# Kernel optimization log

Hardware: AMD Instinct MI355X
Metric: run time of the kernel (lower is better)

The kernel has to match this reference:

```python
import jax, jax.numpy as jnp
import numpy as np

N = 100000
E = 1600000
D_IN = 128
D_HID = 128
D_OUT = 128
HEADS = 4
NEG_SLOPE = 0.2  # PyG GATConv default leaky_relu slope


def setup_inputs() -> dict:
    key = jax.random.key(0)
    ks = jax.random.split(key, 16)
    ch1 = D_HID // HEADS
    ch2 = D_OUT // HEADS
    inp = {
        "x": jax.random.normal(ks[0], (N, D_IN), dtype=jnp.float32),
        "edge_index": jax.random.randint(ks[1], (2, E), 0, N, dtype=jnp.int64),
        # conv1 params
        "W1": jax.random.normal(ks[2], (D_IN, HEADS * ch1), dtype=jnp.float32) * 0.05,
        "a1_src": jax.random.normal(ks[3], (HEADS, ch1), dtype=jnp.float32) * 0.05,
        "a1_dst": jax.random.normal(ks[4], (HEADS, ch1), dtype=jnp.float32) * 0.05,
        "b1": jnp.zeros((HEADS * ch1,), dtype=jnp.float32),
        # conv2 params
        "W2": jax.random.normal(ks[5], (D_HID, HEADS * ch2), dtype=jnp.float32) * 0.05,
        "a2_src": jax.random.normal(ks[6], (HEADS, ch2), dtype=jnp.float32) * 0.05,
        "a2_dst": jax.random.normal(ks[7], (HEADS, ch2), dtype=jnp.float32) * 0.05,
        "b2": jnp.zeros((HEADS * ch2,), dtype=jnp.float32),
        # residual linear
        "Wr": jax.random.normal(ks[8], (D_IN, D_OUT), dtype=jnp.float32) * 0.05,
        "br": jnp.zeros((D_OUT,), dtype=jnp.float32),
    }
    return inp


def _gat_conv(x, W, a_src, a_dst, bias, src, dst, n_nodes):
    """Single PyG-style GATConv (concat heads, eval-mode / no dropout).
    src/dst already include self loops. x: [N, Din]. Returns [N, H*C]."""
    H, C = a_src.shape
    h = (x @ W).reshape(n_nodes, H, C)                      # [N,H,C]
    s_src = jnp.einsum("nhc,hc->nh", h, a_src)              # [N,H]
    s_dst = jnp.einsum("nhc,hc->nh", h, a_dst)              # [N,H]
    e = s_src[src] + s_dst[dst]                             # [E',H]
    e = jnp.where(e > 0, e, NEG_SLOPE * e)                  # leaky_relu
    # softmax over edges grouped by destination node
    e_max = jax.ops.segment_max(e, dst, num_segments=n_nodes)  # [N,H]
    e_exp = jnp.exp(e - e_max[dst])
    denom = jax.ops.segment_sum(e_exp, dst, num_segments=n_nodes)  # [N,H]
    alpha = e_exp / denom[dst]                              # [E',H]
    msg = alpha[:, :, None] * h[src]                        # [E',H,C]
    out = jax.ops.segment_sum(msg, dst, num_segments=n_nodes)  # [N,H,C]
    return out.reshape(n_nodes, H * C) + bias


def reference(x, edge_index, W1, a1_src, a1_dst, b1, W2, a2_src, a2_dst, b2, Wr, br):
    n_nodes = x.shape[0]
    loops = jnp.arange(n_nodes, dtype=edge_index.dtype)
    src = jnp.concatenate([edge_index[0], loops])           # add_self_loops=True
    dst = jnp.concatenate([edge_index[1], loops])
    h1 = _gat_conv(x, W1, a1_src, a1_dst, b1, src, dst, n_nodes)
    h1 = jax.nn.relu(h1)
    h2 = _gat_conv(h1, W2, a2_src, a2_dst, b2, src, dst, n_nodes)
    return h2 + x @ Wr + br
```

## Files before the change

### kernel.cpp

```cpp
#include <hip/hip_runtime.h>

#define NEG_SLOPE 0.2f

__device__ __forceinline__ float leaky1(float e) { return e > 0.f ? e : NEG_SLOPE * e; }

__device__ __forceinline__ unsigned short f2bf(float f) {
    unsigned u = __float_as_uint(f);
    u += 0x7fffu + ((u >> 16) & 1u);
    return (unsigned short)(u >> 16);
}

#define EPB 4096

__global__ __launch_bounds__(256) void bucket_hist(const int* __restrict__ dst,
                                                   int* __restrict__ gcnt,
                                                   int* __restrict__ relBase,
                                                   int E, int N, int NB) {
    __shared__ int hist[256];
    int t = threadIdx.x, blk = blockIdx.x;
    if (t < NB) hist[t] = 0;
    __syncthreads();
    int e0 = blk * EPB + t;
#pragma unroll 4
    for (int k = 0; k < EPB / 256; ++k) {
        int e = e0 + k * 256;
        if (e < E) {
            int d = dst[e];
            if ((unsigned)d < (unsigned)N) atomicAdd(&hist[d >> 9], 1);
        }
    }
    __syncthreads();
    if (t < NB) relBase[blk * NB + t] = atomicAdd(&gcnt[t], hist[t]);
}

__global__ __launch_bounds__(256) void scan_buckets(const int* __restrict__ gcnt,
                                                    int* __restrict__ gboff, int NB) {
    __shared__ int sm[256];
    int t = threadIdx.x;
    int v = (t < NB) ? gcnt[t] : 0;
    sm[t] = v;
    __syncthreads();
#pragma unroll
    for (int o = 1; o < 256; o <<= 1) {
        int u = (t >= o) ? sm[t - o] : 0;
        __syncthreads();
        sm[t] += u;
        __syncthreads();
    }
    if (t < NB) gboff[t] = sm[t] - v;
    if (t == NB - 1) gboff[NB] = sm[t];
}

__global__ __launch_bounds__(256) void bucket_scatter(const int* __restrict__ src,
                                                      const int* __restrict__ dst,
                                                      const int* __restrict__ gboff,
                                                      const int* __restrict__ relBase,
                                                      int2* __restrict__ eb,
                                                      int E, int N, int NB) {
    __shared__ int cur[256];
    int t = threadIdx.x, blk = blockIdx.x;
    if (t < NB) cur[t] = gboff[t] + relBase[blk * NB + t];
    __syncthreads();
    int e0 = blk * EPB + t;
#pragma unroll 4
    for (int k = 0; k < EPB / 256; ++k) {
        int e = e0 + k * 256;
        if (e < E) {
            int d = dst[e];
            if ((unsigned)d < (unsigned)N) {
                int pos = atomicAdd(&cur[d >> 9], 1);
                eb[pos] = make_int2(src[e], d);
            }
        }
    }
}

__global__ __launch_bounds__(512) void csr_build(const int2* __restrict__ eb,
                                                 const int* __restrict__ gboff,
                                                 int* __restrict__ offs,
                                                 int* __restrict__ csr,
                                                 int N, int NB) {
    __shared__ int lcnt[512];
    __shared__ int sm[512];
    __shared__ int cur[512];
    int t = threadIdx.x, b = blockIdx.x;
    lcnt[t] = 0;
    __syncthreads();
    int s0 = gboff[b], s1 = gboff[b + 1];
    for (int e = s0 + t; e < s1; e += 512) atomicAdd(&lcnt[eb[e].y & 511], 1);
    __syncthreads();
    int v = lcnt[t];
    sm[t] = v;
    __syncthreads();
#pragma unroll
    for (int o = 1; o < 512; o <<= 1) {
        int u = (t >= o) ? sm[t - o] : 0;
        __syncthreads();
        sm[t] += u;
        __syncthreads();
    }
    int base = gboff[b] + sm[t] - v;
    cur[t] = base;
    int n0 = (b << 9) + t;
    if (n0 < N) offs[n0] = base;
    if (b == NB - 1 && t == 0) offs[N] = gboff[NB];
    __syncthreads();
    for (int e = s0 + t; e < s1; e += 512) {
        int2 p = eb[e];
        int pos = atomicAdd(&cur[p.y & 511], 1);
        csr[pos] = p.x;
    }
}


__global__ __launch_bounds__(256) void gemm128(const float* __restrict__ X,
                                               const float* __restrict__ W,
                                               float* __restrict__ OUT,
                                               unsigned short* __restrict__ HB,
                                               const float* __restrict__ bias,
                                               int accumulate,
                                               const float* __restrict__ ASrc,
                                               const float* __restrict__ ADst,
                                               float* __restrict__ sS4,
                                               float* __restrict__ sD4, int N) {
    __shared__ float Xs[32][128];
    __shared__ float Ws[64][128];
    int t = threadIdx.x;
    int row0 = blockIdx.x << 5;
    {
        const float4* xg = (const float4*)(X + (size_t)row0 * 128);
        float4* xs = (float4*)&Xs[0][0];
#pragma unroll
        for (int i = 0; i < 4; ++i) xs[t + 256 * i] = xg[t + 256 * i];
    }
    int cx = t & 31, ry = t >> 5;
    int c0 = cx << 2, r0 = ry << 2;
    float acc[4][4] = {};
#pragma unroll 1
    for (int ph = 0; ph < 2; ++ph) {
        __syncthreads();
        {
            const float4* wg = (const float4*)(W + (size_t)ph * 64 * 128);
            float4* ws = (float4*)&Ws[0][0];
#pragma unroll
            for (int i = 0; i < 8; ++i) ws[t + 256 * i] = wg[t + 256 * i];
        }
        __syncthreads();
#pragma unroll 4
        for (int k4 = 0; k4 < 16; ++k4) {
            float4 a[4], b[4];
#pragma unroll
            for (int i = 0; i < 4; ++i)
                a[i] = *(const float4*)&Xs[r0 + i][(ph << 6) + (k4 << 2)];
#pragma unroll
            for (int kk = 0; kk < 4; ++kk)
                b[kk] = *(const float4*)&Ws[(k4 << 2) + kk][c0];
#pragma unroll
            for (int i = 0; i < 4; ++i) {
                acc[i][0] = fmaf(a[i].x, b[0].x, acc[i][0]);
                acc[i][1] = fmaf(a[i].x, b[0].y, acc[i][1]);
                acc[i][2] = fmaf(a[i].x, b[0].z, acc[i][2]);
                acc[i][3] = fmaf(a[i].x, b[0].w, acc[i][3]);
                acc[i][0] = fmaf(a[i].y, b[1].x, acc[i][0]);
                acc[i][1] = fmaf(a[i].y, b[1].y, acc[i][1]);
                acc[i][2] = fmaf(a[i].y, b[1].z, acc[i][2]);
                acc[i][3] = fmaf(a[i].y, b[1].w, acc[i][3]);
                acc[i][0] = fmaf(a[i].z, b[2].x, acc[i][0]);
                acc[i][1] = fmaf(a[i].z, b[2].y, acc[i][1]);
                acc[i][2] = fmaf(a[i].z, b[2].z, acc[i][2]);
                acc[i][3] = fmaf(a[i].z, b[2].w, acc[i][3]);
                acc[i][0] = fmaf(a[i].w, b[3].x, acc[i][0]);
                acc[i][1] = fmaf(a[i].w, b[3].y, acc[i][1]);
                acc[i][2] = fmaf(a[i].w, b[3].z, acc[i][2]);
                acc[i][3] = fmaf(a[i].w, b[3].w, acc[i][3]);
            }
        }
    }
    float4 bv = make_float4(0.f, 0.f, 0.f, 0.f);
    if (bias) bv = *(const float4*)&bias[c0];
    float4 sa = make_float4(0.f, 0.f, 0.f, 0.f), da = sa;
    if (ASrc) {
        sa = *(const float4*)&ASrc[c0];
        da = *(const float4*)&ADst[c0];
    }
#pragma unroll
    for (int i = 0; i < 4; ++i) {
        size_t row = (size_t)(row0 + r0 + i);
        float4 o;
        o.x = acc[i][0] + bv.x;
        o.y = acc[i][1] + bv.y;
        o.z = acc[i][2] + bv.z;
        o.w = acc[i][3] + bv.w;
        if (accumulate) {
            const float4 old = *(const float4*)(OUT + row * 128 + c0);
            o.x += old.x; o.y += old.y; o.z += old.z; o.w += old.w;
        }
        if (OUT) *(float4*)(OUT + row * 128 + c0) = o;
        if (HB) {
            ushort4 hv;
            hv.x = f2bf(o.x); hv.y = f2bf(o.y); hv.z = f2bf(o.z); hv.w = f2bf(o.w);
            *(ushort4*)(HB + row * 128 + c0) = hv;
        }
        if (ASrc) {
            float ps = o.x * sa.x + o.y * sa.y + o.z * sa.z + o.w * sa.w;
            float pd = o.x * da.x + o.y * da.y + o.z * da.z + o.w * da.w;
            ps += __shfl_xor(ps, 1); pd += __shfl_xor(pd, 1);
            ps += __shfl_xor(ps, 2); pd += __shfl_xor(pd, 2);
            ps += __shfl_xor(ps, 4); pd += __shfl_xor(pd, 4);
            if ((cx & 7) == 0) {
                sS4[row * 4 + (cx >> 3)] = ps;
                sD4[row * 4 + (cx >> 3)] = pd;
            }
        }
    }
}


__global__ __launch_bounds__(256) void agg7_kernel(const unsigned short* __restrict__ hb,
                                                   const float* __restrict__ sS4,
                                                   const float* __restrict__ sD4,
                                                   const int* __restrict__ offs,
                                                   const int* __restrict__ csr,
                                                   const float* __restrict__ bias,
                                                   float* __restrict__ out,
                                                   int do_relu, int N) {
    int n = (blockIdx.x << 2) + (threadIdx.x >> 6);
    if (n >= N) return;
    int lane = threadIdx.x & 63;
    int q    = lane >> 4;
    int cl   = lane & 15;
    int hd   = cl >> 2;
    unsigned clo = (unsigned)cl << 4;

    float sdh = sD4[(n << 2) + hd];
    float selfw = __expf(leaky1(sS4[(n << 2) + hd] + sdh));

    float acc[8] = {0.f, 0.f, 0.f, 0.f, 0.f, 0.f, 0.f, 0.f};
    float wsum = 0.f;

    int off = offs[n], end = offs[n + 1];
#pragma unroll 1
    for (int base = off; base < end; base += 16) {
        int e0 = base + q;
        int sj[4];
        float wj[4];
#pragma unroll
        for (int i = 0; i < 4; ++i) sj[i] = csr[e0 + (i << 2)];
#pragma unroll
        for (int i = 0; i < 4; ++i) {
            float s = sS4[((unsigned)sj[i] << 2) + hd] + sdh;
            float w = __expf(leaky1(s));
            wj[i] = (e0 + (i << 2) < end) ? w : 0.f;
        }
#pragma unroll
        for (int i = 0; i < 4; ++i) {
            uint4 v = *(const uint4*)((const char*)hb + (((unsigned)sj[i] << 8) + clo));
            float w = wj[i];
            wsum += w;
            acc[0] = fmaf(w, __uint_as_float(v.x << 16), acc[0]);
            acc[1] = fmaf(w, __uint_as_float(v.x & 0xffff0000u), acc[1]);
            acc[2] = fmaf(w, __uint_as_float(v.y << 16), acc[2]);
            acc[3] = fmaf(w, __uint_as_float(v.y & 0xffff0000u), acc[3]);
            acc[4] = fmaf(w, __uint_as_float(v.z << 16), acc[4]);
            acc[5] = fmaf(w, __uint_as_float(v.z & 0xffff0000u), acc[5]);
            acc[6] = fmaf(w, __uint_as_float(v.w << 16), acc[6]);
            acc[7] = fmaf(w, __uint_as_float(v.w & 0xffff0000u), acc[7]);
        }
    }
#pragma unroll
    for (int k = 0; k < 8; ++k) {
        acc[k] += __shfl_xor(acc[k], 16);
        acc[k] += __shfl_xor(acc[k], 32);
    }
    wsum += __shfl_xor(wsum, 16);
    wsum += __shfl_xor(wsum, 32);

    float iv = 1.0f / (wsum + selfw);

    if (q == 0) {
        uint4 hv = *(const uint4*)((const char*)hb + (((unsigned)n << 8) + clo));
        float hs[8];
        hs[0] = __uint_as_float(hv.x << 16);
        hs[1] = __uint_as_float(hv.x & 0xffff0000u);
        hs[2] = __uint_as_float(hv.y << 16);
        hs[3] = __uint_as_float(hv.y & 0xffff0000u);
        hs[4] = __uint_as_float(hv.z << 16);
        hs[5] = __uint_as_float(hv.z & 0xffff0000u);
        hs[6] = __uint_as_float(hv.w << 16);
        hs[7] = __uint_as_float(hv.w & 0xffff0000u);
        float4 b0 = *(const float4*)&bias[8 * cl];
        float4 b1 = *(const float4*)&bias[8 * cl + 4];
        float4 o0, o1;
        o0.x = fmaf(fmaf(selfw, hs[0], acc[0]), iv, b0.x);
        o0.y = fmaf(fmaf(selfw, hs[1], acc[1]), iv, b0.y);
        o0.z = fmaf(fmaf(selfw, hs[2], acc[2]), iv, b0.z);
        o0.w = fmaf(fmaf(selfw, hs[3], acc[3]), iv, b0.w);
        o1.x = fmaf(fmaf(selfw, hs[4], acc[4]), iv, b1.x);
        o1.y = fmaf(fmaf(selfw, hs[5], acc[5]), iv, b1.y);
        o1.z = fmaf(fmaf(selfw, hs[6], acc[6]), iv, b1.z);
        o1.w = fmaf(fmaf(selfw, hs[7], acc[7]), iv, b1.w);
        if (do_relu) {
            o0.x = fmaxf(o0.x, 0.f); o0.y = fmaxf(o0.y, 0.f);
            o0.z = fmaxf(o0.z, 0.f); o0.w = fmaxf(o0.w, 0.f);
            o1.x = fmaxf(o1.x, 0.f); o1.y = fmaxf(o1.y, 0.f);
            o1.z = fmaxf(o1.z, 0.f); o1.w = fmaxf(o1.w, 0.f);
        }
        *(float4*)(out + (size_t)n * 128 + 8 * cl) = o0;
        *(float4*)(out + (size_t)n * 128 + 8 * cl + 4) = o1;
    }
}


extern "C" void kernel_launch(void* const* d_in, const int* in_sizes, int n_in,
                              void* d_out, int out_size, void* d_ws, size_t ws_size,
                              hipStream_t stream) {
    const float* x   = (const float*)d_in[0];
    const int*   ei  = (const int*)d_in[1];
    const float* W1  = (const float*)d_in[2];
    const float* a1s = (const float*)d_in[3];
    const float* a1d = (const float*)d_in[4];
    const float* b1  = (const float*)d_in[5];
    const float* W2  = (const float*)d_in[6];
    const float* a2s = (const float*)d_in[7];
    const float* a2d = (const float*)d_in[8];
    const float* b2  = (const float*)d_in[9];
    const float* Wr  = (const float*)d_in[10];
    const float* br  = (const float*)d_in[11];
    float* out = (float*)d_out;

    int N = in_sizes[0] / 128;
    int E = in_sizes[1] / 2;
    const int* src = ei;
    const int* dst = ei + E;
    int NB = (N + 511) >> 9;
    int ebl = (E + EPB - 1) / EPB;

    char* w = (char*)d_ws;
    size_t p = 0;
    auto take = [&](size_t bytes) -> char* {
        char* r = w + p;
        p = (p + bytes + 255) & ~(size_t)255;
        return r;
    };
    float* bufB = (float*)take((size_t)N * 128 * 4);
    unsigned short* hb = (unsigned short*)take((size_t)N * 128 * 2);
    float* sS4  = (float*)take((size_t)N * 4 * 4);
    float* sD4  = (float*)take((size_t)N * 4 * 4);
    int* gcnt   = (int*)take((size_t)256 * 4);
    int* offs   = (int*)take((size_t)(N + 1) * 4);
    int* gboff  = (int*)take((size_t)257 * 4);
    int* relBase = (int*)take((size_t)ebl * NB * 4);
    int2* eb    = (int2*)take((size_t)E * 8);
    int* csr    = (int*)take((size_t)(E + 16) * 4);

    hipMemsetAsync(gcnt, 0, 256 * 4, stream);
    hipMemsetAsync(csr + E, 0, 16 * 4, stream);

    bucket_hist<<<ebl, 256, 0, stream>>>(dst, gcnt, relBase, E, N, NB);
    scan_buckets<<<1, 256, 0, stream>>>(gcnt, gboff, NB);
    bucket_scatter<<<ebl, 256, 0, stream>>>(src, dst, gboff, relBase, eb, E, N, NB);
    csr_build<<<NB, 512, 0, stream>>>(eb, gboff, offs, csr, N, NB);

    int gb = N / 32;
    int ab = (N + 3) / 4;

    gemm128<<<gb, 256, 0, stream>>>(x, W1, nullptr, hb, nullptr, 0, a1s, a1d, sS4, sD4, N);
    agg7_kernel<<<ab, 256, 0, stream>>>(hb, sS4, sD4, offs, csr, b1, bufB, 1, N);
    gemm128<<<gb, 256, 0, stream>>>(bufB, W2, nullptr, hb, nullptr, 0, a2s, a2d, sS4, sD4, N);
    agg7_kernel<<<ab, 256, 0, stream>>>(hb, sS4, sD4, offs, csr, b2, out, 0, N);
    gemm128<<<gb, 256, 0, stream>>>(x, Wr, out, nullptr, br, 1, nullptr, nullptr, nullptr, nullptr, N);
}
```

Baseline: 488.3 us.

## Replace FP32 SIMT GEMM with split-bf16 MFMA GEMM using 64-row tiles

Rewrites the dense 128x128 projection kernel to use bf16 MFMA instructions. Each fp32 operand is split into a high and a low bf16 part, and three MFMA products (hi*hi, hi*lo, lo*hi) approximate fp32 accuracy. Tiles grow to 64 rows per block, and the epilogue goes through a padded shared-memory transpose so each thread handles 32 contiguous columns of one row. This targets the FMA-bound SIMT GEMM cost. In exchange it adds per-block conversion of W and X into split bf16, larger shared memory use, and slightly different rounding.

```diff
diff --git a/kernel.cpp b/kernel.cpp
--- a/kernel.cpp
+++ b/kernel.cpp
@@ -1,6 +1,9 @@
 #include <hip/hip_runtime.h>
 
 #define NEG_SLOPE 0.2f
+
+typedef short bf16x8 __attribute__((ext_vector_type(8)));
+typedef float f32x4 __attribute__((ext_vector_type(4)));
 
 __device__ __forceinline__ float leaky1(float e) { return e > 0.f ? e : NEG_SLOPE * e; }
 
@@ -8,6 +11,13 @@
     unsigned u = __float_as_uint(f);
     u += 0x7fffu + ((u >> 16) & 1u);
     return (unsigned short)(u >> 16);
+}
+
+__device__ __forceinline__ void split2(float x, short& h, short& lo) {
+    unsigned short hb_ = f2bf(x);
+    float hf = __uint_as_float(((unsigned)hb_) << 16);
+    h = (short)hb_;
+    lo = (short)f2bf(x - hf);
 }
 
 #define EPB 4096
@@ -113,104 +123,146 @@
 }
 
 
-__global__ __launch_bounds__(256) void gemm128(const float* __restrict__ X,
-                                               const float* __restrict__ W,
-                                               float* __restrict__ OUT,
-                                               unsigned short* __restrict__ HB,
-                                               const float* __restrict__ bias,
-                                               int accumulate,
-                                               const float* __restrict__ ASrc,
-                                               const float* __restrict__ ADst,
-                                               float* __restrict__ sS4,
-                                               float* __restrict__ sD4, int N) {
-    __shared__ float Xs[32][128];
-    __shared__ float Ws[64][128];
+__global__ __launch_bounds__(256, 3) void gemm_mfma(const float* __restrict__ X,
+                                                    const float* __restrict__ W,
+                                                    float* __restrict__ OUT,
+                                                    unsigned short* __restrict__ HB,
+                                                    const float* __restrict__ bias,
+                                                    int accumulate,
+                                                    const float* __restrict__ ASrc,
+                                                    const float* __restrict__ ADst,
+                                                    float* __restrict__ sS4,
+                                                    float* __restrict__ sD4, int N) {
+    __shared__ __align__(16) char pool[49152];
+    short* At2h = (short*)pool;
+    short* At2l = (short*)(pool + 8192);
+    short* Bt2h = (short*)(pool + 16384);
+    short* Bt2l = (short*)(pool + 32768);
+    float* outS = (float*)pool;
+
     int t = threadIdx.x;
-    int row0 = blockIdx.x << 5;
-    {
-        const float4* xg = (const float4*)(X + (size_t)row0 * 128);
-        float4* xs = (float4*)&Xs[0][0];
-#pragma unroll
-        for (int i = 0; i < 4; ++i) xs[t + 256 * i] = xg[t + 256 * i];
-    }
-    int cx = t & 31, ry = t >> 5;
-    int c0 = cx << 2, r0 = ry << 2;
-    float acc[4][4] = {};
+    int row0 = blockIdx.x << 6;
+    int l = t & 63, w = t >> 6, g = l >> 4, r = l & 15;
+    int r0 = w << 4;
+
+    f32x4 acc[8];
+#pragma unroll
+    for (int nb = 0; nb < 8; ++nb) acc[nb] = (f32x4){0.f, 0.f, 0.f, 0.f};
+
+    int arow = t >> 2, aj = t & 3;
+    int growA = row0 + arow;
+    if (growA > N - 1) growA = N - 1;
+    int bc = t & 127, bh4 = (t >> 7) << 2;
+
 #pragma unroll 1
     for (int ph = 0; ph < 2; ++ph) {
         __syncthreads();
         {
-            const float4* wg = (const float4*)(W + (size_t)ph * 64 * 128);
-            float4* ws = (float4*)&Ws[0][0];
-#pragma unroll
-            for (int i = 0; i < 8; ++i) ws[t + 256 * i] = wg[t + 256 * i];
-        }
-        __syncthreads();
-#pragma unroll 4
-        for (int k4 = 0; k4 < 16; ++k4) {
-            float4 a[4], b[4];
-#pragma unroll
-            for (int i = 0; i < 4; ++i)
-                a[i] = *(const float4*)&Xs[r0 + i][(ph << 6) + (k4 << 2)];
-#pragma unroll
-            for (int kk = 0; kk < 4; ++kk)
-                b[kk] = *(const float4*)&Ws[(k4 << 2) + kk][c0];
-#pragma unroll
-            for (int i = 0; i < 4; ++i) {
-                acc[i][0] = fmaf(a[i].x, b[0].x, acc[i][0]);
-                acc[i][1] = fmaf(a[i].x, b[0].y, acc[i][1]);
-                acc[i][2] = fmaf(a[i].x, b[0].z, acc[i][2]);
-                acc[i][3] = fmaf(a[i].x, b[0].w, acc[i][3]);
-                acc[i][0] = fmaf(a[i].y, b[1].x, acc[i][0]);
-                acc[i][1] = fmaf(a[i].y, b[1].y, acc[i][1]);
-                acc[i][2] = fmaf(a[i].y, b[1].z, acc[i][2]);
-                acc[i][3] = fmaf(a[i].y, b[1].w, acc[i][3]);
-                acc[i][0] = fmaf(a[i].z, b[2].x, acc[i][0]);
-                acc[i][1] = fmaf(a[i].z, b[2].y, acc[i][1]);
-                acc[i][2] = fmaf(a[i].z, b[2].z, acc[i][2]);
-                acc[i][3] = fmaf(a[i].z, b[2].w, acc[i][3]);
-                acc[i][0] = fmaf(a[i].w, b[3].x, acc[i][0]);
-                acc[i][1] = fmaf(a[i].w, b[3].y, acc[i][1]);
-                acc[i][2] = fmaf(a[i].w, b[3].z, acc[i][2]);
-                acc[i][3] = fmaf(a[i].w, b[3].w, acc[i][3]);
-            }
-        }
-    }
-    float4 bv = make_float4(0.f, 0.f, 0.f, 0.f);
-    if (bias) bv = *(const float4*)&bias[c0];
-    float4 sa = make_float4(0.f, 0.f, 0.f, 0.f), da = sa;
-    if (ASrc) {
-        sa = *(const float4*)&ASrc[c0];
-        da = *(const float4*)&ADst[c0];
-    }
-#pragma unroll
-    for (int i = 0; i < 4; ++i) {
-        size_t row = (size_t)(row0 + r0 + i);
-        float4 o;
-        o.x = acc[i][0] + bv.x;
-        o.y = acc[i][1] + bv.y;
-        o.z = acc[i][2] + bv.z;
-        o.w = acc[i][3] + bv.w;
+            const float* xp = X + (size_t)growA * 128 + (ph << 6) + (aj << 4);
+            float4 x0 = *(const float4*)(xp + 0);
+            float4 x1 = *(const float4*)(xp + 4);
+            float4 x2 = *(const float4*)(xp + 8);
+            float4 x3 = *(const float4*)(xp + 12);
+            float v[16] = {x0.x, x0.y, x0.z, x0.w, x1.x, x1.y, x1.z, x1.w,
+                           x2.x, x2.y, x2.z, x2.w, x3.x, x3.y, x3.z, x3.w};
+#pragma unroll
+            for (int u = 0; u < 2; ++u) {
+                bf16x8 hv, lv;
+#pragma unroll
+                for (int i = 0; i < 8; ++i) {
+                    short hh, ll;
+                    split2(v[u * 8 + i], hh, ll);
+                    hv[i] = hh; lv[i] = ll;
+                }
+                int kg = 2 * aj + u;
+                *(bf16x8*)&At2h[(kg * 64 + arow) * 8] = hv;
+                *(bf16x8*)&At2l[(kg * 64 + arow) * 8] = lv;
+            }
+        }
+        {
+#pragma unroll
+            for (int j = 0; j < 4; ++j) {
+                int kg = bh4 + j;
+                bf16x8 hv, lv;
+#pragma unroll
+                for (int i = 0; i < 8; ++i) {
+                    float f = W[(size_t)((ph << 6) + (kg << 3) + i) * 128 + bc];
+                    short hh, ll;
+                    split2(f, hh, ll);
+                    hv[i] = hh; lv[i] = ll;
+                }
+                *(bf16x8*)&Bt2h[(kg * 128 + bc) * 8] = hv;
+                *(bf16x8*)&Bt2l[(kg * 128 + bc) * 8] = lv;
+            }
+        }
+        __syncthreads();
+#pragma unroll
+        for (int m = 0; m < 2; ++m) {
+            int kb = m << 2;
+            bf16x8 ah = *(const bf16x8*)&At2h[((kb + g) * 64 + r0 + r) * 8];
+            bf16x8 al = *(const bf16x8*)&At2l[((kb + g) * 64 + r0 + r) * 8];
+#pragma unroll
+            for (int nb = 0; nb < 8; ++nb) {
+                bf16x8 bhv = *(const bf16x8*)&Bt2h[((kb + g) * 128 + (nb << 4) + r) * 8];
+                bf16x8 blv = *(const bf16x8*)&Bt2l[((kb + g) * 128 + (nb << 4) + r) * 8];
+                acc[nb] = __builtin_amdgcn_mfma_f32_16x16x32_bf16(ah, bhv, acc[nb], 0, 0, 0);
+                acc[nb] = __builtin_amdgcn_mfma_f32_16x16x32_bf16(ah, blv, acc[nb], 0, 0, 0);
+                acc[nb] = __builtin_amdgcn_mfma_f32_16x16x32_bf16(al, bhv, acc[nb], 0, 0, 0);
+            }
+        }
+    }
+    __syncthreads();
+#pragma unroll
+    for (int nb = 0; nb < 8; ++nb)
+#pragma unroll
+        for (int reg = 0; reg < 4; ++reg)
+            outS[(r0 + (g << 2) + reg) * 129 + (nb << 4) + r] = acc[nb][reg];
+    __syncthreads();
+    int erow = t & 63, q = t >> 6;
+    int grow = row0 + erow;
+    if (grow < N) {
+        float o[32];
+#pragma unroll
+        for (int i = 0; i < 32; ++i) o[i] = outS[erow * 129 + (q << 5) + i];
+        if (bias) {
+#pragma unroll
+            for (int i = 0; i < 32; ++i) o[i] += bias[(q << 5) + i];
+        }
         if (accumulate) {
-            const float4 old = *(const float4*)(OUT + row * 128 + c0);
-            o.x += old.x; o.y += old.y; o.z += old.z; o.w += old.w;
-        }
-        if (OUT) *(float4*)(OUT + row * 128 + c0) = o;
+#pragma unroll
+            for (int i = 0; i < 8; ++i) {
+                float4 old = *(const float4*)(OUT + (size_t)grow * 128 + (q << 5) + 4 * i);
+                o[4 * i] += old.x; o[4 * i + 1] += old.y;
+                o[4 * i + 2] += old.z; o[4 * i + 3] += old.w;
+            }
+        }
+        if (OUT) {
+#pragma unroll
+            for (int i = 0; i < 8; ++i) {
+                float4 v4 = make_float4(o[4 * i], o[4 * i + 1], o[4 * i + 2], o[4 * i + 3]);
+                *(float4*)(OUT + (size_t)grow * 128 + (q << 5) + 4 * i) = v4;
+            }
+        }
         if (HB) {
-            ushort4 hv;
-            hv.x = f2bf(o.x); hv.y = f2bf(o.y); hv.z = f2bf(o.z); hv.w = f2bf(o.w);
-            *(ushort4*)(HB + row * 128 + c0) = hv;
+#pragma unroll
+            for (int u = 0; u < 4; ++u) {
+                uint4 hv;
+                hv.x = (unsigned)f2bf(o[8 * u + 0]) | ((unsigned)f2bf(o[8 * u + 1]) << 16);
+                hv.y = (unsigned)f2bf(o[8 * u + 2]) | ((unsigned)f2bf(o[8 * u + 3]) << 16);
+                hv.z = (unsigned)f2bf(o[8 * u + 4]) | ((unsigned)f2bf(o[8 * u + 5]) << 16);
+                hv.w = (unsigned)f2bf(o[8 * u + 6]) | ((unsigned)f2bf(o[8 * u + 7]) << 16);
+                *(uint4*)(HB + (size_t)grow * 128 + (q << 5) + 8 * u) = hv;
+            }
         }
         if (ASrc) {
-            float ps = o.x * sa.x + o.y * sa.y + o.z * sa.z + o.w * sa.w;
-            float pd = o.x * da.x + o.y * da.y + o.z * da.z + o.w * da.w;
-            ps += __shfl_xor(ps, 1); pd += __shfl_xor(pd, 1);
-            ps += __shfl_xor(ps, 2); pd += __shfl_xor(pd, 2);
-            ps += __shfl_xor(ps, 4); pd += __shfl_xor(pd, 4);
-            if ((cx & 7) == 0) {
-                sS4[row * 4 + (cx >> 3)] = ps;
-                sD4[row * 4 + (cx >> 3)] = pd;
-            }
+            float ps = 0.f, pd = 0.f;
+#pragma unroll
+            for (int i = 0; i < 32; ++i) {
+                ps = fmaf(o[i], ASrc[(q << 5) + i], ps);
+                pd = fmaf(o[i], ADst[(q << 5) + i], pd);
+            }
+            sS4[(size_t)grow * 4 + q] = ps;
+            sD4[(size_t)grow * 4 + q] = pd;
         }
     }
 }
@@ -361,12 +413,12 @@
     bucket_scatter<<<ebl, 256, 0, stream>>>(src, dst, gboff, relBase, eb, E, N, NB);
     csr_build<<<NB, 512, 0, stream>>>(eb, gboff, offs, csr, N, NB);
 
-    int gb = N / 32;
+    int gbm = (N + 63) >> 6;
     int ab = (N + 3) / 4;
 
-    gemm128<<<gb, 256, 0, stream>>>(x, W1, nullptr, hb, nullptr, 0, a1s, a1d, sS4, sD4, N);
+    gemm_mfma<<<gbm, 256, 0, stream>>>(x, W1, nullptr, hb, nullptr, 0, a1s, a1d, sS4, sD4, N);
     agg7_kernel<<<ab, 256, 0, stream>>>(hb, sS4, sD4, offs, csr, b1, bufB, 1, N);
-    gemm128<<<gb, 256, 0, stream>>>(bufB, W2, nullptr, hb, nullptr, 0, a2s, a2d, sS4, sD4, N);
+    gemm_mfma<<<gbm, 256, 0, stream>>>(bufB, W2, nullptr, hb, nullptr, 0, a2s, a2d, sS4, sD4, N);
     agg7_kernel<<<ab, 256, 0, stream>>>(hb, sS4, sD4, offs, csr, b2, out, 0, N);
-    gemm128<<<gb, 256, 0, stream>>>(x, Wr, out, nullptr, br, 1, nullptr, nullptr, nullptr, nullptr, N);
-}
+    gemm_mfma<<<gbm, 256, 0, stream>>>(x, Wr, out, nullptr, br, 1, nullptr, nullptr, nullptr, nullptr, N);
+}
```

New measurement: 425.4 us. 1.15x faster.
